# Performance work log

Hardware: AMD Instinct MI355X
Metric: run time of the kernel (lower is better)

## Reference

```python
import jax, jax.numpy as jnp
import numpy as np

HK, HV, DK, DV, KW = 16, 32, 128, 128, 4  # key heads, value heads, head dims, conv kernel


def _l2norm(x, eps=1e-6):
    return x * jax.lax.rsqrt(jnp.sum(x * x, axis=-1, keepdims=True) + eps)


def setup_inputs() -> dict:
    key = jax.random.key(0)
    ks = jax.random.split(key, 6)
    B, T = 2, 2048
    C = HK * DK * 2 + HV * DV  # 8192
    return {
        "mixed_qkv": jax.random.normal(ks[0], (B, T, C), dtype=jnp.float32),
        "b": jax.random.normal(ks[1], (B, T, HV), dtype=jnp.float32),
        "a": jax.random.normal(ks[2], (B, T, HV), dtype=jnp.float32),
        "conv_weights": jax.random.normal(ks[3], (C, KW), dtype=jnp.float32) * 0.1,
        "dt_bias": jax.random.normal(ks[4], (HV,), dtype=jnp.float32),
        "A_log": jax.random.normal(ks[5], (HV,), dtype=jnp.float32) * 0.1,
    }


def reference(mixed_qkv, b, a, conv_weights, dt_bias, A_log):
    B, T, C = mixed_qkv.shape
    # --- depthwise causal conv1d (short kernel) + SiLU ---
    xp = jnp.pad(mixed_qkv, ((0, 0), (KW - 1, 0), (0, 0)))
    conv = sum(xp[:, j:j + T, :] * conv_weights[:, j] for j in range(KW))
    x = jax.nn.silu(conv)
    # --- split heads ---
    q = x[..., : HK * DK].reshape(B, T, HK, DK)
    k = x[..., HK * DK: 2 * HK * DK].reshape(B, T, HK, DK)
    v = x[..., 2 * HK * DK:].reshape(B, T, HV, DV)
    q = _l2norm(q)
    k = _l2norm(k)
    rep = HV // HK  # GQA: repeat q,k across value-head groups
    q = jnp.repeat(q, rep, axis=2)
    k = jnp.repeat(k, rep, axis=2)
    beta = jax.nn.sigmoid(b)                                   # [B,T,HV]
    g = -jnp.exp(A_log) * jax.nn.softplus(a + dt_bias)          # [B,T,HV]
    scale = DK ** -0.5
    q = q * scale
    # time-major for scan: [T,B,HV,*]
    qT, kT, vT = (jnp.moveaxis(t, 1, 0) for t in (q, k, v))
    betaT = jnp.moveaxis(beta, 1, 0)
    gT = jnp.moveaxis(g, 1, 0)

    def step(S, inp):
        qt, kt, vt, bt, gt = inp
        S = S * jnp.exp(gt)[..., None, None]                   # gated decay
        kv = jnp.einsum('bhk,bhkv->bhv', kt, S)                # read memory
        delta = (vt - kv) * bt[..., None]                      # delta rule update
        S = S + jnp.einsum('bhk,bhv->bhkv', kt, delta)
        o = jnp.einsum('bhk,bhkv->bhv', qt, S)
        return S, o

    S0 = jnp.zeros((B, HV, DK, DV), dtype=mixed_qkv.dtype)
    _, oT = jax.lax.scan(step, S0, (qT, kT, vT, betaT, gT))
    out = jnp.moveaxis(oT, 0, 1).reshape(B, T, HV * DV)
    return out
```

## Files before the change

kernel.cpp:

```cpp
#include <hip/hip_runtime.h>

#define T_LEN 2048
#define C_LEN 8192
#define NHV   32

__device__ __forceinline__ float frcp(float x) { return __builtin_amdgcn_rcpf(x); }
__device__ __forceinline__ float sigm(float x) { return frcp(1.f + __expf(-x)); }

#define WS_XQK_BYTES 67108864ULL
#define WS_NEED      (WS_XQK_BYTES + 2ULL*NHV*T_LEN*8ULL)

struct F8 { float v[8]; };

__device__ __forceinline__ F8 ld8(const float* p, bool pred) {
  F8 r;
  if (pred) {
    float4 a = *(const float4*)p, b = *(const float4*)(p + 4);
    r.v[0]=a.x; r.v[1]=a.y; r.v[2]=a.z; r.v[3]=a.w;
    r.v[4]=b.x; r.v[5]=b.y; r.v[6]=b.z; r.v[7]=b.w;
  } else {
#pragma unroll
    for (int i = 0; i < 8; ++i) r.v[i] = 0.f;
  }
  return r;
}

__global__ __launch_bounds__(256, 4) void k1_prep(
    const float* __restrict__ xin, const float* __restrict__ win,
    float* __restrict__ xqk)
{
  const int gx  = blockIdx.x;
  const int qk  = gx & 1, tc = (gx >> 1) & 255, b = gx >> 9;
  const int tid = threadIdx.x;
  const int hs  = tid >> 4;
  const int lo  = (tid & 15) * 8;
  const int ch  = qk * 2048 + hs * 128 + lo;

  const float* xb = xin + (size_t)b * T_LEN * C_LEN + ch;

  F8 wt0, wt1, wt2, wt3;
#pragma unroll
  for (int c = 0; c < 8; ++c) {
    float4 w = *(const float4*)(win + (size_t)(ch + c) * 4);
    wt0.v[c] = w.x; wt1.v[c] = w.y; wt2.v[c] = w.z; wt3.v[c] = w.w;
  }

  const int t0 = tc * 8;
  F8 r0 = ld8(xb + (size_t)(t0 - 3) * C_LEN, t0 >= 3);
  F8 r1 = ld8(xb + (size_t)(t0 - 2) * C_LEN, t0 >= 2);
  F8 r2 = ld8(xb + (size_t)(t0 - 1) * C_LEN, t0 >= 1);

  float* outp = xqk + ((size_t)(b * 16 + hs) * T_LEN) * 256 + qk * 128 + lo;
  const float qscale = qk ? 1.f : 0.08838834764831845f;

#pragma unroll
  for (int dt = 0; dt < 8; ++dt) {
    const int t = t0 + dt;
    F8 cur = ld8(xb + (size_t)t * C_LEN, true);
    F8 y; float sq = 0.f;
#pragma unroll
    for (int c = 0; c < 8; ++c) {
      float s = wt0.v[c]*r0.v[c] + wt1.v[c]*r1.v[c] + wt2.v[c]*r2.v[c] + wt3.v[c]*cur.v[c];
      s = s * sigm(s);
      y.v[c] = s; sq += s * s;
    }
    sq += __shfl_xor(sq, 1); sq += __shfl_xor(sq, 2);
    sq += __shfl_xor(sq, 4); sq += __shfl_xor(sq, 8);
    const float rn = rsqrtf(sq + 1e-6f) * qscale;
    float4 oa, ob;
    oa.x=y.v[0]*rn; oa.y=y.v[1]*rn; oa.z=y.v[2]*rn; oa.w=y.v[3]*rn;
    ob.x=y.v[4]*rn; ob.y=y.v[5]*rn; ob.z=y.v[6]*rn; ob.w=y.v[7]*rn;
    float* op = outp + (size_t)t * 256;
    *(float4*)op = oa; *(float4*)(op + 4) = ob;
    r0 = r1; r1 = r2; r2 = cur;
  }
}

__global__ __launch_bounds__(256) void k1b_gate(
    const float* __restrict__ bin, const float* __restrict__ ain,
    const float* __restrict__ dtb, const float* __restrict__ alg,
    float2* __restrict__ xgb)
{
  const int idx = blockIdx.x * 256 + threadIdx.x;
  const int b = idx >> 16, hv = (idx >> 11) & 31, t = idx & 2047;
  const size_t src = ((size_t)(b * T_LEN + t)) * NHV + hv;
  const float bt = sigm(bin[src]);
  const float x  = ain[src] + dtb[hv];
  const float sp = fmaxf(x, 0.f) + log1pf(__expf(-fabsf(x)));
  xgb[idx] = make_float2(__expf(-__expf(alg[hv]) * sp), bt);
}

__global__ __launch_bounds__(256, 4) void k2_scan(
    const float* __restrict__ xin, const float* __restrict__ win,
    const float* __restrict__ xqk, const float2* __restrict__ xgb,
    float* __restrict__ out)
{
  const int bx = blockIdx.x;
  const int chunk = bx & 15, hv = (bx >> 4) & 31, bb = bx >> 9;
  const int hk = hv >> 1;
  const int tid = threadIdx.x;
  const int i  = tid & 31;
  const int cc = tid >> 5;
  const int vch = 4096 + hv * 128 + chunk * 8 + cc;

  __shared__ float opT[32 * 257];
  __shared__ float vs[32][8];

  const float*  qkp = xqk + ((size_t)(bb * 16 + hk) * T_LEN) * 256;
  const float2* gbp = xgb + ((size_t)(bb * NHV + hv)) * T_LEN;
  const float*  xvb = xin + (size_t)bb * T_LEN * C_LEN + vch;
  const float4  wv  = *(const float4*)(win + (size_t)vch * 4);
  float* outp = out + (size_t)bb * T_LEN * 4096 + hv * 128 + chunk * 8;

  float S0 = 0.f, S1 = 0.f, S2 = 0.f, S3 = 0.f;

  for (int t0 = 0; t0 < T_LEN; t0 += 32) {
    {
      const int t = t0 + i;
      const float* p = xvb + (size_t)t * C_LEN;
      float a0 = (t >= 3) ? p[-3 * C_LEN] : 0.f;
      float a1 = (t >= 2) ? p[-2 * C_LEN] : 0.f;
      float a2 = (t >= 1) ? p[-1 * C_LEN] : 0.f;
      float a3 = p[0];
      float s = wv.x*a0 + wv.y*a1 + wv.z*a2 + wv.w*a3;
      vs[i][cc] = s * sigm(s);
    }
    __syncthreads();

    const float* qrow = qkp + (size_t)t0 * 256;
#pragma unroll 4
    for (int tt = 0; tt < 32; ++tt) {
      const float4 kf = *(const float4*)(qrow + 128 + i * 4);
      const float4 qf = *(const float4*)(qrow + i * 4);
      const float  vv = vs[tt][cc];
      const float2 gb = gbp[t0 + tt];

      float dk = kf.x*S0 + kf.y*S1 + kf.z*S2 + kf.w*S3;
      dk += __shfl_xor(dk, 1); dk += __shfl_xor(dk, 2);
      dk += __shfl_xor(dk, 4); dk += __shfl_xor(dk, 8);
      dk += __shfl_xor(dk, 16);

      const float eg    = gb.x;
      const float delta = (vv - eg * dk) * gb.y;

      S0 = eg*S0 + kf.x*delta; S1 = eg*S1 + kf.y*delta;
      S2 = eg*S2 + kf.z*delta; S3 = eg*S3 + kf.w*delta;

      const float o = qf.x*S0 + qf.y*S1 + qf.z*S2 + qf.w*S3;
      opT[i * 257 + tt * 8 + cc] = o;
      qrow += 256;
    }
    __syncthreads();

    {
      float s = 0.f;
#pragma unroll
      for (int r = 0; r < 32; ++r) s += opT[r * 257 + tid];
      const int tt2 = tid >> 3, c2 = tid & 7;
      outp[(size_t)(t0 + tt2) * 4096 + c2] = s;
    }
  }
}

#define TILE  32
#define NCOL  16
#define XSS   276
#define OTS   33

__global__ __launch_bounds__(256) void gdn_fused(
    const float* __restrict__ xin, const float* __restrict__ bin,
    const float* __restrict__ ain, const float* __restrict__ win,
    const float* __restrict__ dtb, const float* __restrict__ alg,
    float* __restrict__ out)
{
  const int tid   = threadIdx.x;
  const int bx    = blockIdx.x;
  const int chunk = bx & 7;
  const int hv    = (bx >> 3) & 31;
  const int bb    = bx >> 8;
  const int hk    = hv >> 1;

  const int qch0 = hk * 128;
  const int kch0 = 2048 + hk * 128;
  const int vch0 = 4096 + hv * 128 + chunk * NCOL;

  __shared__ __align__(16) float  xs[TILE][XSS];
  __shared__ __align__(16) float4 wc[272];
  __shared__ float  opT[256 * OTS];
  __shared__ float2 s_gb[TILE];
  __shared__ float  s_rq[TILE], s_rk[TILE];

  for (int i = tid; i < 272; i += 256) {
    int gch = (i < 128) ? (qch0 + i) : (i < 256) ? (kch0 + i - 128) : (vch0 + i - 256);
    wc[i] = *(const float4*)(win + (size_t)gch * 4);
  }

  const int lane = tid & 63;
  const int wv   = tid >> 6;
  const int rg   = lane & 15;
  const int col  = wv * 4 + (lane >> 4);
  const int rg4  = rg * 4;

  const float dtbv = dtb[hv];
  const float nA   = -__expf(alg[hv]);

  float S[8];
#pragma unroll
  for (int m = 0; m < 8; ++m) S[m] = 0.f;

  const float* xb  = xin + (size_t)bb * T_LEN * C_LEN;
  float*       op  = out + (size_t)bb * T_LEN * 4096 + hv * 128 + chunk * NCOL;
  float*       opw = &opT[(wv * 64 + lane) * OTS];

  for (int t0 = 0; t0 < T_LEN; t0 += TILE) {
    __syncthreads();
    for (int idx = tid; idx < TILE * 68; idx += 256) {
      int row = idx / 68;
      int c4  = idx - row * 68;
      int gch = (c4 < 32) ? (qch0 + c4 * 4)
              : (c4 < 64) ? (kch0 + (c4 - 32) * 4)
                          : (vch0 + (c4 - 64) * 4);
      int r = t0 + row - 3;
      const float* gp = xb + (size_t)r * C_LEN + gch;
      float4 a0 = (r     >= 0) ? *(const float4*)(gp)             : make_float4(0,0,0,0);
      float4 a1 = (r + 1 >= 0) ? *(const float4*)(gp + C_LEN)     : make_float4(0,0,0,0);
      float4 a2 = (r + 2 >= 0) ? *(const float4*)(gp + 2 * C_LEN) : make_float4(0,0,0,0);
      float4 a3 =                *(const float4*)(gp + 3 * C_LEN);
      float4 w0 = wc[c4 * 4], w1 = wc[c4 * 4 + 1], w2 = wc[c4 * 4 + 2], w3 = wc[c4 * 4 + 3];
      float4 o4;
      o4.x = a0.x * w0.x + a1.x * w0.y + a2.x * w0.z + a3.x * w0.w;
      o4.y = a0.y * w1.x + a1.y * w1.y + a2.y * w1.z + a3.y * w1.w;
      o4.z = a0.z * w2.x + a1.z * w2.y + a2.z * w2.z + a3.z * w2.w;
      o4.w = a0.w * w3.x + a1.w * w3.y + a2.w * w3.z + a3.w * w3.w;
      o4.x *= sigm(o4.x); o4.y *= sigm(o4.y); o4.z *= sigm(o4.z); o4.w *= sigm(o4.w);
      *(float4*)&xs[row][c4 * 4] = o4;
    }
    if (tid < TILE) {
      int tg = t0 + tid;
      size_t boff = ((size_t)bb * T_LEN + tg) * NHV + hv;
      float  bt = sigm(bin[boff]);
      float  x  = ain[boff] + dtbv;
      float  sp = fmaxf(x, 0.f) + log1pf(__expf(-fabsf(x)));
      s_gb[tid] = make_float2(__expf(nA * sp), bt);
    }
    __syncthreads();
    {
      int ttn = tid >> 3, l8 = tid & 7;
      float sq = 0.f, sk = 0.f;
#pragma unroll
      for (int m = 0; m < 16; ++m) {
        int cc = m * 8 + l8;
        float aq = xs[ttn][cc];
        float ak = xs[ttn][128 + cc];
        sq += aq * aq; sk += ak * ak;
      }
      sq += __shfl_xor(sq, 1); sq += __shfl_xor(sq, 2); sq += __shfl_xor(sq, 4);
      sk += __shfl_xor(sk, 1); sk += __shfl_xor(sk, 2); sk += __shfl_xor(sk, 4);
      if (l8 == 0) {
        s_rq[ttn] = rsqrtf(sq + 1e-6f) * 0.08838834764831845f;
        s_rk[ttn] = rsqrtf(sk + 1e-6f);
      }
    }
    __syncthreads();
    for (int idx = tid; idx < TILE * 64; idx += 256) {
      int row = idx >> 6, c4 = idx & 63;
      float f = (c4 < 32) ? s_rq[row] : s_rk[row];
      float4* p = (float4*)&xs[row][c4 * 4];
      float4 v = *p;
      v.x *= f; v.y *= f; v.z *= f; v.w *= f;
      *p = v;
    }
    __syncthreads();
#pragma unroll 2
    for (int tt = 0; tt < TILE; ++tt) {
      const float* xr = &xs[tt][0];
      float4 k0 = *(const float4*)(xr + 128 + rg4);
      float4 k1 = *(const float4*)(xr + 192 + rg4);
      float  vv = xr[256 + col];
      float4 q0 = *(const float4*)(xr +       rg4);
      float4 q1 = *(const float4*)(xr +  64 + rg4);

      float dk = k0.x*S[0] + k0.y*S[1] + k0.z*S[2] + k0.w*S[3]
               + k1.x*S[4] + k1.y*S[5] + k1.z*S[6] + k1.w*S[7];
      dk += __shfl_xor(dk, 1); dk += __shfl_xor(dk, 2);
      dk += __shfl_xor(dk, 4); dk += __shfl_xor(dk, 8);

      float2 gb    = s_gb[tt];
      float  eg    = gb.x;
      float  delta = (vv - eg * dk) * gb.y;

      S[0] = eg*S[0] + k0.x*delta;  S[1] = eg*S[1] + k0.y*delta;
      S[2] = eg*S[2] + k0.z*delta;  S[3] = eg*S[3] + k0.w*delta;
      S[4] = eg*S[4] + k1.x*delta;  S[5] = eg*S[5] + k1.y*delta;
      S[6] = eg*S[6] + k1.z*delta;  S[7] = eg*S[7] + k1.w*delta;

      float o = q0.x*S[0] + q0.y*S[1] + q0.z*S[2] + q0.w*S[3]
              + q1.x*S[4] + q1.y*S[5] + q1.z*S[6] + q1.w*S[7];
      opw[tt] = o;
    }
    __syncthreads();
    {
      int ttb = tid & 31, colb = tid >> 5;
#pragma unroll
      for (int it = 0; it < 2; ++it) {
        int cc = colb + it * 8;
        const float* pp = &opT[(cc * 16) * OTS + ttb];
        float s = 0.f;
#pragma unroll
        for (int i = 0; i < 16; ++i) s += pp[i * OTS];
        op[(size_t)(t0 + ttb) * 4096 + cc] = s;
      }
    }
  }
}

extern "C" void kernel_launch(void* const* d_in, const int* in_sizes, int n_in,
                              void* d_out, int out_size, void* d_ws, size_t ws_size,
                              hipStream_t stream) {
  (void)in_sizes; (void)n_in; (void)out_size;
  const float* xin = (const float*)d_in[0];
  const float* bin = (const float*)d_in[1];
  const float* ain = (const float*)d_in[2];
  const float* win = (const float*)d_in[3];
  const float* dtb = (const float*)d_in[4];
  const float* alg = (const float*)d_in[5];
  float* out = (float*)d_out;

  if (ws_size >= WS_NEED) {
    float*  xqk = (float*)d_ws;
    float2* xgb = (float2*)((char*)d_ws + WS_XQK_BYTES);
    k1_prep<<<dim3(1024), dim3(256), 0, stream>>>(xin, win, xqk);
    k1b_gate<<<dim3(512), dim3(256), 0, stream>>>(bin, ain, dtb, alg, xgb);
    k2_scan<<<dim3(1024), dim3(256), 0, stream>>>(xin, win, xqk, xgb, out);
  } else {
    gdn_fused<<<dim3(512), dim3(256), 0, stream>>>(xin, bin, ain, win, dtb, alg, out);
  }
}
```

Baseline: 948.7 us.

## Precompute v conv into output buffer and restructure scan to 16-lane DPP reductions

The prep kernel now also computes the conv+SiLU for the v channels and writes them into the output buffer, so the scan kernel no longer recomputes the v convolution. The scan kernel is restructured so that each 16-lane row owns one value column with 8 state elements per lane, and it reduces with DPP row sums instead of the LDS transpose and block syncs. This removes shared memory and barriers from the scan and halves the number of blocks. In exchange it writes the output in place at every step with a single lane storing, and it trades occupancy for more per-thread state.

New measurement: 1.063 ms. 1.12x slower.

```diff
diff --git a/kernel.cpp b/kernel.cpp
--- a/kernel.cpp
+++ b/kernel.cpp
@@ -6,6 +6,19 @@
 
 __device__ __forceinline__ float frcp(float x) { return __builtin_amdgcn_rcpf(x); }
 __device__ __forceinline__ float sigm(float x) { return frcp(1.f + __expf(-x)); }
+
+template<int CTRL>
+__device__ __forceinline__ float dpp_mov(float x) {
+  int yi = __builtin_amdgcn_update_dpp(0, __builtin_bit_cast(int, x), CTRL, 0xf, 0xf, true);
+  return __builtin_bit_cast(float, yi);
+}
+__device__ __forceinline__ float row_sum16(float x) {
+  x += dpp_mov<0xB1>(x);
+  x += dpp_mov<0x4E>(x);
+  x += dpp_mov<0x124>(x);
+  x += dpp_mov<0x128>(x);
+  return x;
+}
 
 #define WS_XQK_BYTES 67108864ULL
 #define WS_NEED      (WS_XQK_BYTES + 2ULL*NHV*T_LEN*8ULL)
@@ -27,14 +40,14 @@
 
 __global__ __launch_bounds__(256, 4) void k1_prep(
     const float* __restrict__ xin, const float* __restrict__ win,
-    float* __restrict__ xqk)
+    float* __restrict__ xqk, float* __restrict__ xv )
 {
   const int gx  = blockIdx.x;
-  const int qk  = gx & 1, tc = (gx >> 1) & 255, b = gx >> 9;
+  const int seg = gx & 3, tc = (gx >> 2) & 255, b = gx >> 10;
   const int tid = threadIdx.x;
   const int hs  = tid >> 4;
   const int lo  = (tid & 15) * 8;
-  const int ch  = qk * 2048 + hs * 128 + lo;
+  const int ch  = seg * 2048 + hs * 128 + lo;
 
   const float* xb = xin + (size_t)b * T_LEN * C_LEN + ch;
 
@@ -50,8 +63,12 @@
   F8 r1 = ld8(xb + (size_t)(t0 - 2) * C_LEN, t0 >= 2);
   F8 r2 = ld8(xb + (size_t)(t0 - 1) * C_LEN, t0 >= 1);
 
-  float* outp = xqk + ((size_t)(b * 16 + hs) * T_LEN) * 256 + qk * 128 + lo;
-  const float qscale = qk ? 1.f : 0.08838834764831845f;
+  const bool isqk = (seg < 2);
+  float* outp = isqk
+      ? xqk + ((size_t)(b * 16 + hs) * T_LEN) * 256 + seg * 128 + lo
+      : xv  + ((size_t)b * T_LEN) * 4096 + (seg - 2) * 2048 + hs * 128 + lo;
+  const size_t ostride = isqk ? 256 : 4096;
+  const float qscale = (seg == 0) ? 0.08838834764831845f : 1.f;
 
 #pragma unroll
   for (int dt = 0; dt < 8; ++dt) {
@@ -64,13 +81,15 @@
       s = s * sigm(s);
       y.v[c] = s; sq += s * s;
     }
-    sq += __shfl_xor(sq, 1); sq += __shfl_xor(sq, 2);
-    sq += __shfl_xor(sq, 4); sq += __shfl_xor(sq, 8);
-    const float rn = rsqrtf(sq + 1e-6f) * qscale;
+    float rn = 1.f;
+    if (isqk) {
+      sq = row_sum16(sq);
+      rn = rsqrtf(sq + 1e-6f) * qscale;
+    }
     float4 oa, ob;
     oa.x=y.v[0]*rn; oa.y=y.v[1]*rn; oa.z=y.v[2]*rn; oa.w=y.v[3]*rn;
     ob.x=y.v[4]*rn; ob.y=y.v[5]*rn; ob.z=y.v[6]*rn; ob.w=y.v[7]*rn;
-    float* op = outp + (size_t)t * 256;
+    float* op = outp + (size_t)t * ostride;
     *(float4*)op = oa; *(float4*)(op + 4) = ob;
     r0 = r1; r1 = r2; r2 = cur;
   }
@@ -90,75 +109,51 @@
   xgb[idx] = make_float2(__expf(-__expf(alg[hv]) * sp), bt);
 }
 
-__global__ __launch_bounds__(256, 4) void k2_scan(
-    const float* __restrict__ xin, const float* __restrict__ win,
+__global__ __launch_bounds__(256, 2) void k2_scan(
     const float* __restrict__ xqk, const float2* __restrict__ xgb,
-    float* __restrict__ out)
+    float* __restrict__ outv)
 {
   const int bx = blockIdx.x;
-  const int chunk = bx & 15, hv = (bx >> 4) & 31, bb = bx >> 9;
+  const int chunk = bx & 7, hv = (bx >> 3) & 31, bb = bx >> 8;
   const int hk = hv >> 1;
   const int tid = threadIdx.x;
-  const int i  = tid & 31;
-  const int cc = tid >> 5;
-  const int vch = 4096 + hv * 128 + chunk * 8 + cc;
-
-  __shared__ float opT[32 * 257];
-  __shared__ float vs[32][8];
-
-  const float*  qkp = xqk + ((size_t)(bb * 16 + hk) * T_LEN) * 256;
+  const int rg = tid & 15;
+  const int cc = tid >> 4;
+  const int vcol = hv * 128 + chunk * 16 + cc;
+
+  const float*  qk0 = xqk + ((size_t)(bb * 16 + hk) * T_LEN) * 256 + rg * 8;
   const float2* gbp = xgb + ((size_t)(bb * NHV + hv)) * T_LEN;
-  const float*  xvb = xin + (size_t)bb * T_LEN * C_LEN + vch;
-  const float4  wv  = *(const float4*)(win + (size_t)vch * 4);
-  float* outp = out + (size_t)bb * T_LEN * 4096 + hv * 128 + chunk * 8;
-
-  float S0 = 0.f, S1 = 0.f, S2 = 0.f, S3 = 0.f;
-
-  for (int t0 = 0; t0 < T_LEN; t0 += 32) {
-    {
-      const int t = t0 + i;
-      const float* p = xvb + (size_t)t * C_LEN;
-      float a0 = (t >= 3) ? p[-3 * C_LEN] : 0.f;
-      float a1 = (t >= 2) ? p[-2 * C_LEN] : 0.f;
-      float a2 = (t >= 1) ? p[-1 * C_LEN] : 0.f;
-      float a3 = p[0];
-      float s = wv.x*a0 + wv.y*a1 + wv.z*a2 + wv.w*a3;
-      vs[i][cc] = s * sigm(s);
-    }
-    __syncthreads();
-
-    const float* qrow = qkp + (size_t)t0 * 256;
+  float*        vop = outv + (size_t)bb * T_LEN * 4096 + vcol;
+
+  float S0=0.f,S1=0.f,S2=0.f,S3=0.f,S4=0.f,S5=0.f,S6=0.f,S7=0.f;
+
 #pragma unroll 4
-    for (int tt = 0; tt < 32; ++tt) {
-      const float4 kf = *(const float4*)(qrow + 128 + i * 4);
-      const float4 qf = *(const float4*)(qrow + i * 4);
-      const float  vv = vs[tt][cc];
-      const float2 gb = gbp[t0 + tt];
-
-      float dk = kf.x*S0 + kf.y*S1 + kf.z*S2 + kf.w*S3;
-      dk += __shfl_xor(dk, 1); dk += __shfl_xor(dk, 2);
-      dk += __shfl_xor(dk, 4); dk += __shfl_xor(dk, 8);
-      dk += __shfl_xor(dk, 16);
-
-      const float eg    = gb.x;
-      const float delta = (vv - eg * dk) * gb.y;
-
-      S0 = eg*S0 + kf.x*delta; S1 = eg*S1 + kf.y*delta;
-      S2 = eg*S2 + kf.z*delta; S3 = eg*S3 + kf.w*delta;
-
-      const float o = qf.x*S0 + qf.y*S1 + qf.z*S2 + qf.w*S3;
-      opT[i * 257 + tt * 8 + cc] = o;
-      qrow += 256;
-    }
-    __syncthreads();
-
-    {
-      float s = 0.f;
-#pragma unroll
-      for (int r = 0; r < 32; ++r) s += opT[r * 257 + tid];
-      const int tt2 = tid >> 3, c2 = tid & 7;
-      outp[(size_t)(t0 + tt2) * 4096 + c2] = s;
-    }
+  for (int t = 0; t < T_LEN; ++t) {
+    const float* qr = qk0 + (size_t)t * 256;
+    const float4 ka = *(const float4*)(qr + 128);
+    const float4 kb = *(const float4*)(qr + 132);
+    const float4 qa = *(const float4*)(qr);
+    const float4 qb = *(const float4*)(qr + 4);
+    const float  vv = vop[(size_t)t * 4096];
+    const float2 gb = gbp[t];
+
+    float d0 = ka.x*S0 + ka.y*S1 + ka.z*S2 + ka.w*S3;
+    float d1 = kb.x*S4 + kb.y*S5 + kb.z*S6 + kb.w*S7;
+    float dk = row_sum16(d0 + d1);
+
+    const float eg    = gb.x;
+    const float delta = (vv - eg * dk) * gb.y;
+
+    S0 = eg*S0 + ka.x*delta; S1 = eg*S1 + ka.y*delta;
+    S2 = eg*S2 + ka.z*delta; S3 = eg*S3 + ka.w*delta;
+    S4 = eg*S4 + kb.x*delta; S5 = eg*S5 + kb.y*delta;
+    S6 = eg*S6 + kb.z*delta; S7 = eg*S7 + kb.w*delta;
+
+    float o0 = qa.x*S0 + qa.y*S1 + qa.z*S2 + qa.w*S3;
+    float o1 = qb.x*S4 + qb.y*S5 + qb.z*S6 + qb.w*S7;
+    float o  = row_sum16(o0 + o1);
+
+    if (rg == 0) vop[(size_t)t * 4096] = o;
   }
 }
 
@@ -329,9 +324,9 @@
   if (ws_size >= WS_NEED) {
     float*  xqk = (float*)d_ws;
     float2* xgb = (float2*)((char*)d_ws + WS_XQK_BYTES);
-    k1_prep<<<dim3(1024), dim3(256), 0, stream>>>(xin, win, xqk);
+    k1_prep<<<dim3(2048), dim3(256), 0, stream>>>(xin, win, xqk, out);
     k1b_gate<<<dim3(512), dim3(256), 0, stream>>>(bin, ain, dtb, alg, xgb);
-    k2_scan<<<dim3(1024), dim3(256), 0, stream>>>(xin, win, xqk, xgb, out);
+    k2_scan<<<dim3(512), dim3(256), 0, stream>>>(xqk, xgb, out);
   } else {
     gdn_fused<<<dim3(512), dim3(256), 0, stream>>>(xin, bin, ain, win, dtb, alg, out);
   }
```
